# Performance work log

Hardware: AMD Instinct MI355X
Metric: run time of the kernel (lower is better)

## Reference

```python
import jax, jax.numpy as jnp
import numpy as np

B, C, L, K, R = 32, 64, 16384, 3, 8

def _lrelu(x):
    return jnp.where(x >= 0, x, 0.1 * x)

def setup_inputs() -> dict:
    key = jax.random.key(0)
    ks = jax.random.split(key, 8)
    s = lambda i, shape: (jax.random.normal(ks[i], shape, jnp.float32) * 0.05)
    return {
        "x0": jax.random.normal(ks[0], (B, C, L), jnp.float32),
        "x1": jax.random.normal(ks[1], (B, 64), jnp.float32),
        "W1": s(2, (64, 64)),           # Linear(64,64).weight [out,in]
        "W2": s(3, (64 * K, 64)),       # Linear(64,64*K).weight
        "conv_w": s(4, (C, C)),         # 1x1 Conv1d weight [out,in]
        "conv_b": s(5, (C,)),
        "ca_w1": s(6, (C // R, C)),     # CA conv1 weight
        "ca_w2": s(7, (C, C // R)),     # CA conv2 weight
    }

def reference(x0, x1, W1, W2, conv_w, conv_b, ca_w1, ca_w2):
    b, c, l = x0.shape
    k = W2.shape[0] // 64
    pad = (k - 1) // 2
    # dynamic per-(b,c) depthwise kernels
    h = _lrelu(x1 @ W1.T)                         # [b,64]
    kern = (h @ W2.T).reshape(b, c, k)            # [b,c,k]
    # depthwise conv1d (cross-correlation), groups=b*c
    xp = jnp.pad(x0, ((0, 0), (0, 0), (pad, pad)))
    out = sum(xp[:, :, j:j + l] * kern[:, :, j:j + 1] for j in range(k))
    out = _lrelu(out)
    # 1x1 conv
    out = jnp.einsum('bcl,oc->bol', out, conv_w) + conv_b[None, :, None]
    # channel attention gate on x1
    att = jax.nn.sigmoid(_lrelu(x1 @ ca_w1.T) @ ca_w2.T)  # [b,c]
    return out + x0 * att[:, :, None]
```

## Files before the change

kernel.cpp:

```cpp
#include <hip/hip_runtime.h>
#include <math.h>

#define B_ 32
#define C_ 64
#define L_ 16384
#define LT 32
#define NT 16
#define NBUF 3
#define NBLK (B_ * (L_ / (LT * NT)))

typedef __attribute__((ext_vector_type(8))) short short8;
typedef __attribute__((ext_vector_type(4))) float f32x4;

__device__ __forceinline__ unsigned short f2bf(float x) {
  unsigned int u = __builtin_bit_cast(unsigned int, x);
  u += 0x7fffu + ((u >> 16) & 1u);
  return (unsigned short)(u >> 16);
}

__device__ __forceinline__ float lrelu(float x) {
  return x >= 0.f ? x : 0.1f * x;
}

__device__ __forceinline__ void load_lds_16(const void* g, void* l) {
  __builtin_amdgcn_global_load_lds(
      (const __attribute__((address_space(1))) void*)g,
      (__attribute__((address_space(3))) void*)l, 16, 0, 0);
}

__global__ void da_prep(const float* __restrict__ x1,
                        const float* __restrict__ W1,
                        const float* __restrict__ W2,
                        const float* __restrict__ ca_w1,
                        const float* __restrict__ ca_w2,
                        const float* __restrict__ conv_w,
                        float* __restrict__ kern4,
                        float* __restrict__ att,
                        unsigned short* __restrict__ wfrag) {
  int b = blockIdx.x;
  int t = threadIdx.x;
  __shared__ float x1s[64], h[64], a1[8];
  x1s[t] = x1[b * 64 + t];
  __syncthreads();
  {
    const float* w1r = W1 + t * 64;
    float s = 0.f;
    #pragma unroll
    for (int i = 0; i < 64; ++i) s = fmaf(x1s[i], w1r[i], s);
    h[t] = lrelu(s);
  }
  if (t < 8) {
    const float* cw = ca_w1 + t * 64;
    float a = 0.f;
    #pragma unroll
    for (int i = 0; i < 64; ++i) a = fmaf(x1s[i], cw[i], a);
    a1[t] = lrelu(a);
  }
  __syncthreads();
  #pragma unroll
  for (int kk = 0; kk < 3; ++kk) {
    const float* w2r = W2 + (t * 3 + kk) * 64;
    float s2 = 0.f;
    #pragma unroll
    for (int i = 0; i < 64; ++i) s2 = fmaf(h[i], w2r[i], s2);
    kern4[(b * 64 + t) * 4 + kk] = s2;
  }
  kern4[(b * 64 + t) * 4 + 3] = 0.f;
  {
    float a = 0.f;
    #pragma unroll
    for (int r = 0; r < 8; ++r) a = fmaf(a1[r], ca_w2[t * 8 + r], a);
    att[b * 64 + t] = 1.f / (1.f + expf(-a));
  }
  if (b == 0) {
    #pragma unroll
    for (int kt = 0; kt < 2; ++kt)
      #pragma unroll
      for (int mt = 0; mt < 4; ++mt)
        #pragma unroll
        for (int j = 0; j < 8; ++j) {
          float e = conv_w[(mt * 16 + (t & 15)) * 64 + kt * 32 + (t >> 4) * 8 + j];
          wfrag[(((kt * 4 + mt) * 64) + t) * 8 + j] = f2bf(e);
        }
  }
}

__global__ __launch_bounds__(256, 4) void da_main(
    const float* __restrict__ x0,
    const float* __restrict__ conv_b,
    const float* __restrict__ kern4,
    const float* __restrict__ att,
    const unsigned short* __restrict__ wfrag,
    float* __restrict__ out) {
  __shared__ float x0s[NBUF][64 * LT];
  __shared__ unsigned short midT[LT * 64];
  __shared__ float haloL[2][64];

  int bid = blockIdx.x;
  int b = bid >> 5;
  int base_l = (bid & 31) * (NT * LT);
  int tid = threadIdx.x;
  int lane = tid & 63;
  int wave = tid >> 6;

  int m_lane = lane & 15;
  int qq = lane >> 4;
  int kbase = qq * 8;
  int oh = wave >> 1;
  int lh = wave & 1;
  int wl = lh * 16 + m_lane;

  const float* xb = x0 + (size_t)(b * 64) * L_;

  auto STAGE = [&](int t1, int dd) {
    #pragma unroll
    for (int i = 0; i < 2; ++i) {
      int rg = (wave * 2 + i) * 8;
      int c = rg + (lane >> 3);
      int g = (lane & 7) ^ (c & 7);
      const float* gp = xb + (size_t)c * L_ + base_l + t1 * LT + g * 4;
      load_lds_16(gp, &x0s[dd][rg * LT]);
    }
  };

  short8 af[2][2];
  #pragma unroll
  for (int kt = 0; kt < 2; ++kt)
    #pragma unroll
    for (int mt2 = 0; mt2 < 2; ++mt2)
      af[kt][mt2] =
          *(const short8*)&wfrag[(((kt * 4 + oh * 2 + mt2) * 64) + lane) * 8];

  float4 kv = *(const float4*)&kern4[(b * 64 + lane) * 4];
  float k0 = kv.x, k1 = kv.y, k2 = kv.z;

  float cb_r[2][4], at_r[2][4];
  #pragma unroll
  for (int mt2 = 0; mt2 < 2; ++mt2)
    #pragma unroll
    for (int r = 0; r < 4; ++r) {
      int o = oh * 32 + mt2 * 16 + qq * 4 + r;
      cb_r[mt2][r] = conv_b[o];
      at_r[mt2][r] = att[b * 64 + o];
    }

  float hl0 = 0.f, hnL = 0.f;
  if (wave == 0 && base_l > 0) hl0 = xb[(size_t)lane * L_ + base_l - 1];
  if (wave == 3 && base_l + NT * LT < L_)
    hnL = xb[(size_t)lane * L_ + base_l + NT * LT];
  if (wave == 0) haloL[0][lane] = hl0;

  __syncthreads();

  STAGE(0, 0);
  STAGE(1, 1);

  int cur = 0, nxt = 1, nx2 = 2;
  for (int t = 0; t < NT; ++t) {
    if (t + 2 < NT) STAGE(t + 2, nx2);

    if (t == 0)
      asm volatile("s_waitcnt vmcnt(2)" ::: "memory");
    else if (t < NT - 2)
      asm volatile("s_waitcnt vmcnt(10)" ::: "memory");
    else if (t == NT - 2)
      asm volatile("s_waitcnt vmcnt(8)" ::: "memory");
    __builtin_amdgcn_s_barrier();

    {
      int c = lane;
      int cs = c & 7;
      const float* row = &x0s[cur][c * LT];

      float4 q0 = *(const float4*)&row[((wave * 2 + 0) ^ cs) << 2];
      float4 q1 = *(const float4*)&row[((wave * 2 + 1) ^ cs) << 2];

      float prev, nxtv;
      if (wave == 0) {
        prev = (t == 0) ? hl0 : haloL[t & 1][c];
      } else {
        prev = row[(((wave * 2 - 1) ^ cs) << 2) + 3];
      }
      if (wave == 3) {
        nxtv = (t == NT - 1) ? hnL : x0s[nxt][c * LT + (cs << 2)];
      } else {
        nxtv = row[((wave * 2 + 2) ^ cs) << 2];
      }
      if (wave == 3 && t + 1 < NT) haloL[(t + 1) & 1][c] = q1.w;

      float m0 = fmaf(k0, prev, fmaf(k1, q0.x, k2 * q0.y));
      float m1 = fmaf(k0, q0.x, fmaf(k1, q0.y, k2 * q0.z));
      float m2 = fmaf(k0, q0.y, fmaf(k1, q0.z, k2 * q0.w));
      float m3 = fmaf(k0, q0.z, fmaf(k1, q0.w, k2 * q1.x));
      float m4 = fmaf(k0, q0.w, fmaf(k1, q1.x, k2 * q1.y));
      float m5 = fmaf(k0, q1.x, fmaf(k1, q1.y, k2 * q1.z));
      float m6 = fmaf(k0, q1.y, fmaf(k1, q1.z, k2 * q1.w));
      float m7 = fmaf(k0, q1.z, fmaf(k1, q1.w, k2 * nxtv));

      int lb = wave * 8;
      midT[(lb + 0) * 64 + (c ^ (0 << 3))] = f2bf(lrelu(m0));
      midT[(lb + 1) * 64 + (c ^ (1 << 3))] = f2bf(lrelu(m1));
      midT[(lb + 2) * 64 + (c ^ (2 << 3))] = f2bf(lrelu(m2));
      midT[(lb + 3) * 64 + (c ^ (3 << 3))] = f2bf(lrelu(m3));
      midT[(lb + 4) * 64 + (c ^ (4 << 3))] = f2bf(lrelu(m4));
      midT[(lb + 5) * 64 + (c ^ (5 << 3))] = f2bf(lrelu(m5));
      midT[(lb + 6) * 64 + (c ^ (6 << 3))] = f2bf(lrelu(m6));
      midT[(lb + 7) * 64 + (c ^ (7 << 3))] = f2bf(lrelu(m7));
    }

    float xv[2][4];
    #pragma unroll
    for (int mt2 = 0; mt2 < 2; ++mt2)
      #pragma unroll
      for (int r = 0; r < 4; ++r) {
        int o = oh * 32 + mt2 * 16 + qq * 4 + r;
        xv[mt2][r] =
            x0s[cur][o * LT + (((wl >> 2) ^ (o & 7)) << 2) + (wl & 3)];
      }

    asm volatile("s_waitcnt lgkmcnt(0)" ::: "memory");
    __builtin_amdgcn_s_barrier();

    f32x4 acc[2];
    acc[0] = (f32x4){0.f, 0.f, 0.f, 0.f};
    acc[1] = (f32x4){0.f, 0.f, 0.f, 0.f};
    #pragma unroll
    for (int kt = 0; kt < 2; ++kt) {
      int cb = kt * 32 + kbase;
      const short8 bf =
          *(const short8*)&midT[wl * 64 + (cb ^ ((wl & 7) << 3))];
      acc[0] = __builtin_amdgcn_mfma_f32_16x16x32_bf16(af[kt][0], bf, acc[0],
                                                       0, 0, 0);
      acc[1] = __builtin_amdgcn_mfma_f32_16x16x32_bf16(af[kt][1], bf, acc[1],
                                                       0, 0, 0);
    }

    {
      size_t obase = (size_t)(b * 64) * L_ + base_l + t * LT + wl;
      #pragma unroll
      for (int mt2 = 0; mt2 < 2; ++mt2)
        #pragma unroll
        for (int r = 0; r < 4; ++r) {
          int o = oh * 32 + mt2 * 16 + qq * 4 + r;
          out[obase + (size_t)o * L_] =
              acc[mt2][r] + cb_r[mt2][r] + xv[mt2][r] * at_r[mt2][r];
        }
    }

    int tmp = cur; cur = nxt; nxt = nx2; nx2 = tmp;
  }
}

extern "C" void kernel_launch(void* const* d_in, const int* in_sizes, int n_in,
                              void* d_out, int out_size, void* d_ws, size_t ws_size,
                              hipStream_t stream) {
  const float* x0     = (const float*)d_in[0];
  const float* x1     = (const float*)d_in[1];
  const float* W1     = (const float*)d_in[2];
  const float* W2     = (const float*)d_in[3];
  const float* conv_w = (const float*)d_in[4];
  const float* conv_b = (const float*)d_in[5];
  const float* ca_w1  = (const float*)d_in[6];
  const float* ca_w2  = (const float*)d_in[7];
  float* out = (float*)d_out;

  float* kern4 = (float*)d_ws;
  float* att   = kern4 + B_ * C_ * 4;
  unsigned short* wfrag = (unsigned short*)(att + B_ * C_);

  da_prep<<<dim3(B_), dim3(64), 0, stream>>>(x1, W1, W2, ca_w1, ca_w2, conv_w,
                                             kern4, att, wfrag);
  da_main<<<dim3(NBLK), dim3(256), 0, stream>>>(x0, conv_b, kern4, att, wfrag,
                                                out);
}
```

Before: 63.80 us.

## Repartition MFMA tiles per wave and stage outputs through LDS for float4 stores

Each wave now owns 16 output channels across both 16-column halves, instead of 32 channels over one half. Results are written to a per-wave swizzled LDS slab and read back so each lane issues two coalesced float4 global stores instead of eight scalar stores. Fewer outstanding stores lets the vmcnt waits tighten from 10/8 to 4/2. This adds LDS traffic and shared memory, which may reduce occupancy. It also relies on the wave-local slab needing no barrier.

Result: no change. 63.13 us (median of 2 runs) (-1.0%).

```diff
diff --git a/kernel.cpp b/kernel.cpp
--- a/kernel.cpp
+++ b/kernel.cpp
@@ -94,6 +94,7 @@
     float* __restrict__ out) {
   __shared__ float x0s[NBUF][64 * LT];
   __shared__ unsigned short midT[LT * 64];
+  __shared__ float slab[4 * 16 * 32];
   __shared__ float haloL[2][64];
 
   int bid = blockIdx.x;
@@ -106,9 +107,6 @@
   int m_lane = lane & 15;
   int qq = lane >> 4;
   int kbase = qq * 8;
-  int oh = wave >> 1;
-  int lh = wave & 1;
-  int wl = lh * 16 + m_lane;
 
   const float* xb = x0 + (size_t)(b * 64) * L_;
 
@@ -123,26 +121,21 @@
     }
   };
 
-  short8 af[2][2];
+  short8 af[2];
   #pragma unroll
   for (int kt = 0; kt < 2; ++kt)
-    #pragma unroll
-    for (int mt2 = 0; mt2 < 2; ++mt2)
-      af[kt][mt2] =
-          *(const short8*)&wfrag[(((kt * 4 + oh * 2 + mt2) * 64) + lane) * 8];
+    af[kt] = *(const short8*)&wfrag[(((kt * 4 + wave) * 64) + lane) * 8];
 
   float4 kv = *(const float4*)&kern4[(b * 64 + lane) * 4];
   float k0 = kv.x, k1 = kv.y, k2 = kv.z;
 
-  float cb_r[2][4], at_r[2][4];
+  float cb_r[4], at_r[4];
   #pragma unroll
-  for (int mt2 = 0; mt2 < 2; ++mt2)
-    #pragma unroll
-    for (int r = 0; r < 4; ++r) {
-      int o = oh * 32 + mt2 * 16 + qq * 4 + r;
-      cb_r[mt2][r] = conv_b[o];
-      at_r[mt2][r] = att[b * 64 + o];
-    }
+  for (int r = 0; r < 4; ++r) {
+    int o = wave * 16 + qq * 4 + r;
+    cb_r[r] = conv_b[o];
+    at_r[r] = att[b * 64 + o];
+  }
 
   float hl0 = 0.f, hnL = 0.f;
   if (wave == 0 && base_l > 0) hl0 = xb[(size_t)lane * L_ + base_l - 1];
@@ -155,16 +148,20 @@
   STAGE(0, 0);
   STAGE(1, 1);
 
-  int cur = 0, nxt = 1, nx2 = 2;
+  int o2 = lane >> 2;
+  int lc = lane & 3;
+  int slw = wave * 512;
+
+  int cur = 0, nx1 = 1, nx2 = 2;
   for (int t = 0; t < NT; ++t) {
     if (t + 2 < NT) STAGE(t + 2, nx2);
 
     if (t == 0)
       asm volatile("s_waitcnt vmcnt(2)" ::: "memory");
     else if (t < NT - 2)
-      asm volatile("s_waitcnt vmcnt(10)" ::: "memory");
+      asm volatile("s_waitcnt vmcnt(4)" ::: "memory");
     else if (t == NT - 2)
-      asm volatile("s_waitcnt vmcnt(8)" ::: "memory");
+      asm volatile("s_waitcnt vmcnt(2)" ::: "memory");
     __builtin_amdgcn_s_barrier();
 
     {
@@ -182,7 +179,7 @@
         prev = row[(((wave * 2 - 1) ^ cs) << 2) + 3];
       }
       if (wave == 3) {
-        nxtv = (t == NT - 1) ? hnL : x0s[nxt][c * LT + (cs << 2)];
+        nxtv = (t == NT - 1) ? hnL : x0s[nx1][c * LT + (cs << 2)];
       } else {
         nxtv = row[((wave * 2 + 2) ^ cs) << 2];
       }
@@ -210,12 +207,13 @@
 
     float xv[2][4];
     #pragma unroll
-    for (int mt2 = 0; mt2 < 2; ++mt2)
+    for (int lh = 0; lh < 2; ++lh)
       #pragma unroll
       for (int r = 0; r < 4; ++r) {
-        int o = oh * 32 + mt2 * 16 + qq * 4 + r;
-        xv[mt2][r] =
-            x0s[cur][o * LT + (((wl >> 2) ^ (o & 7)) << 2) + (wl & 3)];
+        int o = wave * 16 + qq * 4 + r;
+        int l = lh * 16 + m_lane;
+        xv[lh][r] =
+            x0s[cur][o * LT + (((l >> 2) ^ (o & 7)) << 2) + (l & 3)];
       }
 
     asm volatile("s_waitcnt lgkmcnt(0)" ::: "memory");
@@ -227,27 +225,38 @@
     #pragma unroll
     for (int kt = 0; kt < 2; ++kt) {
       int cb = kt * 32 + kbase;
-      const short8 bf =
-          *(const short8*)&midT[wl * 64 + (cb ^ ((wl & 7) << 3))];
-      acc[0] = __builtin_amdgcn_mfma_f32_16x16x32_bf16(af[kt][0], bf, acc[0],
-                                                       0, 0, 0);
-      acc[1] = __builtin_amdgcn_mfma_f32_16x16x32_bf16(af[kt][1], bf, acc[1],
-                                                       0, 0, 0);
-    }
+      #pragma unroll
+      for (int lh = 0; lh < 2; ++lh) {
+        int l = lh * 16 + m_lane;
+        const short8 bf =
+            *(const short8*)&midT[l * 64 + (cb ^ ((l & 7) << 3))];
+        acc[lh] = __builtin_amdgcn_mfma_f32_16x16x32_bf16(af[kt], bf, acc[lh],
+                                                          0, 0, 0);
+      }
+    }
+
+    #pragma unroll
+    for (int lh = 0; lh < 2; ++lh)
+      #pragma unroll
+      for (int r = 0; r < 4; ++r) {
+        int op = qq * 4 + r;
+        int l = lh * 16 + m_lane;
+        slab[slw + op * 32 + (l ^ ((op & 7) << 2))] =
+            acc[lh][r] + cb_r[r] + xv[lh][r] * at_r[r];
+      }
 
     {
-      size_t obase = (size_t)(b * 64) * L_ + base_l + t * LT + wl;
-      #pragma unroll
-      for (int mt2 = 0; mt2 < 2; ++mt2)
-        #pragma unroll
-        for (int r = 0; r < 4; ++r) {
-          int o = oh * 32 + mt2 * 16 + qq * 4 + r;
-          out[obase + (size_t)o * L_] =
-              acc[mt2][r] + cb_r[mt2][r] + xv[mt2][r] * at_r[mt2][r];
-        }
-    }
-
-    int tmp = cur; cur = nxt; nxt = nx2; nx2 = tmp;
+      size_t orow = (size_t)(b * 64 + wave * 16 + o2) * L_ + base_l + t * LT;
+      #pragma unroll
+      for (int h = 0; h < 2; ++h) {
+        int l = h * 16 + lc * 4;
+        float4 v =
+            *(const float4*)&slab[slw + o2 * 32 + (l ^ ((o2 & 7) << 2))];
+        *(float4*)&out[orow + l] = v;
+      }
+    }
+
+    int tmp = cur; cur = nx1; nx1 = nx2; nx2 = tmp;
   }
 }
 
```
